# Kernel optimization log

Hardware: AMD Instinct MI355X
Metric: run time of the kernel (lower is better)

Reference implementation:

```python
import jax, jax.numpy as jnp
import numpy as np

B, S, D = 4, 1024, 1024
H = 16
DH = D // H           # 64
ROT = 64              # rotary_emb_dim (full head dim)
NEG_INF = -10000.0
ROPE_BASE = 10000.0


def _rope_tables(seqlen, rot_dim, dtype=jnp.float32):
    inv_freq = 1.0 / (ROPE_BASE ** (jnp.arange(0, rot_dim, 2, dtype=jnp.float32) / rot_dim))
    t = jnp.arange(seqlen, dtype=jnp.float32)
    freqs = jnp.einsum('s,f->sf', t, inv_freq)  # (S, rot_dim//2)
    return jnp.cos(freqs).astype(dtype), jnp.sin(freqs).astype(dtype)


def _apply_rotary(x, cos, sin):
    # x: (B, S, H, DH); GPT-NeoX (non-interleaved) rotary over first ROT dims
    half = ROT // 2
    x_rot, x_pass = x[..., :ROT], x[..., ROT:]
    x1, x2 = x_rot[..., :half], x_rot[..., half:]
    c = cos[None, :, None, :]
    s = sin[None, :, None, :]
    rot = jnp.concatenate([x1 * c - x2 * s, x2 * c + x1 * s], axis=-1)
    return jnp.concatenate([rot, x_pass], axis=-1) if x_pass.shape[-1] else rot


def setup_inputs() -> dict:
    key = jax.random.key(0)
    ks = jax.random.split(key, 5)
    sc_in = 1.0 / np.sqrt(D)
    return {
        'x': jax.random.normal(ks[0], (B, S, D), jnp.float32),
        'Wqkv': jax.random.normal(ks[1], (3 * D, D), jnp.float32) * sc_in,
        'bqkv': jax.random.normal(ks[2], (3 * D,), jnp.float32) * 0.01,
        'Wout': jax.random.normal(ks[3], (D, D), jnp.float32) * sc_in,
        'bout': jax.random.normal(ks[4], (D,), jnp.float32) * 0.01,
    }


def reference(x, Wqkv, bqkv, Wout, bout):
    # QKV projection: (B,S,D) -> (B,S,3,H,DH)
    qkv = (jnp.einsum('bsd,ed->bse', x, Wqkv) + bqkv).reshape(B, S, 3, H, DH)
    q, k, v = qkv[:, :, 0], qkv[:, :, 1], qkv[:, :, 2]
    cos, sin = _rope_tables(S, ROT, q.dtype)
    q = _apply_rotary(q, cos, sin)
    k = _apply_rotary(k, cos, sin)
    scale = 1.0 / np.sqrt(DH)
    scores = jnp.einsum('bthd,bshd->bhts', q, k * scale)  # (B,H,S,S)
    causal_mask = jnp.triu(jnp.full((S, S), NEG_INF, dtype=scores.dtype), 1)
    scores = scores + causal_mask
    attn = jax.nn.softmax(scores, axis=-1)
    out = jnp.einsum('bhts,bshd->bthd', attn, v).reshape(B, S, D)
    return jnp.einsum('bsd,ed->bse', out, Wout) + bout
```

## Files before the change

kernel.cpp:

```cpp
#include <hip/hip_runtime.h>

#define B_ 4
#define S_ 1024
#define D_ 1024
#define H_ 16
#define DH_ 64

typedef unsigned short u16;
typedef __attribute__((ext_vector_type(8))) short bf16x8;
typedef __attribute__((ext_vector_type(4))) float f32x4;

__device__ __forceinline__ float bf2f(u16 h){
  union { unsigned u; float f; } x; x.u = ((unsigned)h) << 16; return x.f;
}
__device__ __forceinline__ u16 f2bf(float f){
  union { float f; unsigned u; } x; x.f = f;
  unsigned u = x.u;
  return (u16)((u + 0x7fffu + ((u >> 16) & 1u)) >> 16);
}

__device__ __forceinline__ void gload16(const u16* g, u16* l){
  __builtin_amdgcn_global_load_lds(
      (const __attribute__((address_space(1))) unsigned int*)g,
      (__attribute__((address_space(3))) unsigned int*)l, 16, 0, 0);
}

__global__ __launch_bounds__(256) void cast3(
    const float* __restrict__ a, u16* __restrict__ oa, int na,
    const float* __restrict__ b, u16* __restrict__ ob, int nb,
    const float* __restrict__ c, u16* __restrict__ oc){
  int i = (blockIdx.x * 256 + threadIdx.x) * 4;
  const float* src; u16* dst;
  if (i < na){ src = a + i; dst = oa + i; }
  else if (i < na + nb){ src = b + (i - na); dst = ob + (i - na); }
  else { src = c + (i - na - nb); dst = oc + (i - na - nb); }
  float4 v = *(const float4*)src;
  union { u16 s[4]; uint2 u; } o;
  o.s[0] = f2bf(v.x); o.s[1] = f2bf(v.y); o.s[2] = f2bf(v.z); o.s[3] = f2bf(v.w);
  *(uint2*)dst = o.u;
}

__global__ __launch_bounds__(256) void rope_tab(float2* __restrict__ tab){
  int idx = blockIdx.x * 256 + threadIdx.x;
  int s = idx >> 5, i = idx & 31;
  float invf = powf(10000.0f, -(float)i * (1.0f / 32.0f));
  float sn, cs;
  sincosf((float)s * invf, &sn, &cs);
  tab[idx] = make_float2(cs, sn);
}

__global__ __launch_bounds__(512, 2) void gemm_qkv8(const u16* __restrict__ A,
    const u16* __restrict__ Bm, const float* __restrict__ bias,
    const float2* __restrict__ tab,
    u16* __restrict__ qb, u16* __restrict__ kb, u16* __restrict__ vb){
  __shared__ u16 As_[2][2][128*64];
  __shared__ u16 Bs_[2][2][128*64];
  const int K = 1024;
  const int tid = threadIdx.x;
  const int lane = tid & 63, wid = tid >> 6;
  const int wr = wid >> 2, wc = wid & 3;
  const int lo = lane & 15, g = lane >> 4;

  const int bid = blockIdx.x;
  const int swz = (bid & 7) * 24 + (bid >> 3);
  const int bx = swz & 15, by = swz >> 4;
  const int m0 = bx * 256, n0 = by * 256;

  f32x4 acc[8][4];
  #pragma unroll
  for (int i = 0; i < 8; ++i)
    #pragma unroll
    for (int j = 0; j < 4; ++j) acc[i][j] = (f32x4){0.f, 0.f, 0.f, 0.f};

  auto stage = [&](int b, int kt){
    const u16* ga = A + (size_t)m0 * K + kt * 64;
    const u16* gb = Bm + (size_t)n0 * K + kt * 64;
    #pragma unroll
    for (int it = 0; it < 2; ++it){
      int c = tid + it * 512;
      int r = c >> 3;
      int colbs = ((c & 7) * 16) ^ ((r & 7) << 4);
      int src = r * K + (colbs >> 1);
      gload16(ga + src,           &As_[b][0][c * 8]);
      gload16(ga + 128*K + src,   &As_[b][1][c * 8]);
      gload16(gb + src,           &Bs_[b][0][c * 8]);
      gload16(gb + 128*K + src,   &Bs_[b][1][c * 8]);
    }
  };

  auto rdA = [&](int b, int qm, int fm, int ks) -> bf16x8 {
    int row = qm*64 + fm*16 + lo;
    int byte = row*128 + ((ks*64 + g*16) ^ ((lo & 7) << 4));
    return *(const bf16x8*)(&As_[b][wr][byte >> 1]);
  };
  auto rdB = [&](int b, int qn, int fn, int ks) -> bf16x8 {
    int row = (wc & 1)*64 + qn*32 + fn*16 + lo;
    int byte = row*128 + ((ks*64 + g*16) ^ ((lo & 7) << 4));
    return *(const bf16x8*)(&Bs_[b][wc >> 1][byte >> 1]);
  };

  auto ktile = [&](int b, int stage_t){
    bf16x8 a[8], bq[4];
    #pragma unroll
    for (int fm = 0; fm < 4; ++fm)
      #pragma unroll
      for (int ks = 0; ks < 2; ++ks) a[fm*2+ks] = rdA(b, 0, fm, ks);
    #pragma unroll
    for (int fn = 0; fn < 2; ++fn)
      #pragma unroll
      for (int ks = 0; ks < 2; ++ks) bq[fn*2+ks] = rdB(b, 0, fn, ks);
    __builtin_amdgcn_s_setprio(1);
    #pragma unroll
    for (int fm = 0; fm < 4; ++fm)
      #pragma unroll
      for (int fn = 0; fn < 2; ++fn)
        #pragma unroll
        for (int ks = 0; ks < 2; ++ks)
          acc[fm][fn] = __builtin_amdgcn_mfma_f32_16x16x32_bf16(a[fm*2+ks], bq[fn*2+ks], acc[fm][fn], 0, 0, 0);
    __builtin_amdgcn_s_setprio(0);
    #pragma unroll
    for (int fn = 0; fn < 2; ++fn)
      #pragma unroll
      for (int ks = 0; ks < 2; ++ks) bq[fn*2+ks] = rdB(b, 1, fn, ks);
    __builtin_amdgcn_s_setprio(1);
    #pragma unroll
    for (int fm = 0; fm < 4; ++fm)
      #pragma unroll
      for (int fn = 0; fn < 2; ++fn)
        #pragma unroll
        for (int ks = 0; ks < 2; ++ks)
          acc[fm][2+fn] = __builtin_amdgcn_mfma_f32_16x16x32_bf16(a[fm*2+ks], bq[fn*2+ks], acc[fm][2+fn], 0, 0, 0);
    __builtin_amdgcn_s_setprio(0);
    #pragma unroll
    for (int fm = 0; fm < 4; ++fm)
      #pragma unroll
      for (int ks = 0; ks < 2; ++ks) a[fm*2+ks] = rdA(b, 1, fm, ks);
    #pragma unroll
    for (int fn = 0; fn < 2; ++fn)
      #pragma unroll
      for (int ks = 0; ks < 2; ++ks) bq[fn*2+ks] = rdB(b, 0, fn, ks);
    __builtin_amdgcn_s_setprio(1);
    #pragma unroll
    for (int fm = 0; fm < 4; ++fm)
      #pragma unroll
      for (int fn = 0; fn < 2; ++fn)
        #pragma unroll
        for (int ks = 0; ks < 2; ++ks)
          acc[4+fm][fn] = __builtin_amdgcn_mfma_f32_16x16x32_bf16(a[fm*2+ks], bq[fn*2+ks], acc[4+fm][fn], 0, 0, 0);
    __builtin_amdgcn_s_setprio(0);
    #pragma unroll
    for (int fn = 0; fn < 2; ++fn)
      #pragma unroll
      for (int ks = 0; ks < 2; ++ks) bq[fn*2+ks] = rdB(b, 1, fn, ks);
    asm volatile("s_waitcnt lgkmcnt(0)" ::: "memory");
    __builtin_amdgcn_sched_barrier(0);
    __builtin_amdgcn_s_barrier();
    __builtin_amdgcn_sched_barrier(0);
    if (stage_t >= 0) stage(b, stage_t);
    __builtin_amdgcn_s_setprio(1);
    #pragma unroll
    for (int fm = 0; fm < 4; ++fm)
      #pragma unroll
      for (int fn = 0; fn < 2; ++fn)
        #pragma unroll
        for (int ks = 0; ks < 2; ++ks)
          acc[4+fm][2+fn] = __builtin_amdgcn_mfma_f32_16x16x32_bf16(a[fm*2+ks], bq[fn*2+ks], acc[4+fm][2+fn], 0, 0, 0);
    __builtin_amdgcn_s_setprio(0);
  };

  stage(0, 0);
  stage(1, 1);
  for (int t = 0; t < 14; ++t){
    asm volatile("s_waitcnt vmcnt(8)" ::: "memory");
    __builtin_amdgcn_s_barrier();
    __builtin_amdgcn_sched_barrier(0);
    ktile(t & 1, t + 2);
  }
  asm volatile("s_waitcnt vmcnt(8)" ::: "memory");
  __builtin_amdgcn_s_barrier();
  __builtin_amdgcn_sched_barrier(0);
  ktile(0, -1);
  asm volatile("s_waitcnt vmcnt(0)" ::: "memory");
  __builtin_amdgcn_s_barrier();
  __builtin_amdgcn_sched_barrier(0);
  ktile(1, -1);

  const int ty = by >> 2;
  const int h  = (by & 3) * 4 + wc;
  float bv[4];
  #pragma unroll
  for (int fn = 0; fn < 4; ++fn) bv[fn] = bias[n0 + wc*64 + fn*16 + lo];

  if (ty < 2){
    u16* dst = (ty == 0) ? qb : kb;
    #pragma unroll
    for (int fm = 0; fm < 8; ++fm){
      #pragma unroll
      for (int j = 0; j < 4; ++j){
        int row = m0 + wr*128 + fm*16 + g*4 + j;
        int bb = row >> 10, s = row & 1023;
        size_t obase = (((size_t)(bb * H_ + h)) * S_ + s) * DH_;
        #pragma unroll
        for (int fn = 0; fn < 2; ++fn){
          int i = fn*16 + lo;
          float2 t2 = tab[s*32 + i];
          float v1 = acc[fm][fn][j] + bv[fn];
          float v2 = acc[fm][fn+2][j] + bv[fn+2];
          dst[obase + i]      = f2bf(v1 * t2.x - v2 * t2.y);
          dst[obase + i + 32] = f2bf(v2 * t2.x + v1 * t2.y);
        }
      }
    }
  } else {
    #pragma unroll
    for (int fm = 0; fm < 8; ++fm){
      #pragma unroll
      for (int j = 0; j < 4; ++j){
        int row = m0 + wr*128 + fm*16 + g*4 + j;
        int bb = row >> 10, s = row & 1023;
        size_t obase = (((size_t)(bb * H_ + h)) * S_ + s) * DH_;
        #pragma unroll
        for (int fn = 0; fn < 4; ++fn)
          vb[obase + fn*16 + lo] = f2bf(acc[fm][fn][j] + bv[fn]);
      }
    }
  }
}

template<int OUT_BF16>
__global__ __launch_bounds__(256) void gemm_bt(const u16* __restrict__ A,
    const u16* __restrict__ Bm, const float* __restrict__ bias,
    void* __restrict__ Cout, int M, int N, int K){
  __shared__ u16 As[2][128*32];
  __shared__ u16 Bs[2][128*32];
  const int tid = threadIdx.x;
  const int lane = tid & 63;
  const int w = tid >> 6;
  const int wr = w >> 1, wc = w & 1;
  const int lo = lane & 15, g = lane >> 4;
  const int m0 = blockIdx.x * 128, n0 = blockIdx.y * 128;

  f32x4 acc[4][4];
  #pragma unroll
  for (int i = 0; i < 4; ++i)
    #pragma unroll
    for (int j = 0; j < 4; ++j) acc[i][j] = (f32x4){0.f, 0.f, 0.f, 0.f};

  const int nt = K >> 5;

  auto stage = [&](int buf, int kt){
    const u16* ga = A + (size_t)m0 * K + kt * 32;
    const u16* gb = Bm + (size_t)n0 * K + kt * 32;
    #pragma unroll
    for (int it = 0; it < 2; ++it){
      int chunk = tid + it * 256;
      int row = chunk >> 2;
      int c0 = (chunk & 3) * 8;
      gload16(ga + (size_t)row * K + c0, &As[buf][chunk * 8]);
      gload16(gb + (size_t)row * K + c0, &Bs[buf][chunk * 8]);
    }
  };

  stage(0, 0);
  __syncthreads();
  int buf = 0;
  for (int kt = 0; kt < nt; ++kt){
    if (kt + 1 < nt) stage(buf ^ 1, kt + 1);
    bf16x8 af[4], bfr[4];
    #pragma unroll
    for (int mi = 0; mi < 4; ++mi)
      af[mi] = *(const bf16x8*)(&As[buf][(wr*64 + mi*16 + lo)*32 + g*8]);
    #pragma unroll
    for (int ni = 0; ni < 4; ++ni)
      bfr[ni] = *(const bf16x8*)(&Bs[buf][(wc*64 + ni*16 + lo)*32 + g*8]);
    #pragma unroll
    for (int mi = 0; mi < 4; ++mi)
      #pragma unroll
      for (int ni = 0; ni < 4; ++ni)
        acc[mi][ni] = __builtin_amdgcn_mfma_f32_16x16x32_bf16(af[mi], bfr[ni], acc[mi][ni], 0, 0, 0);
    __syncthreads();
    buf ^= 1;
  }

  #pragma unroll
  for (int mi = 0; mi < 4; ++mi){
    int row = m0 + wr*64 + mi*16 + g*4;
    #pragma unroll
    for (int ni = 0; ni < 4; ++ni){
      int col = n0 + wc*64 + ni*16 + lo;
      float bvs = bias[col];
      #pragma unroll
      for (int j = 0; j < 4; ++j){
        float v = acc[mi][ni][j] + bvs;
        if (OUT_BF16) ((u16*)Cout)[(size_t)(row + j) * N + col] = f2bf(v);
        else          ((float*)Cout)[(size_t)(row + j) * N + col] = v;
      }
    }
  }
}

__global__ __launch_bounds__(256) void vtrans(const u16* __restrict__ vb,
                                              u16* __restrict__ vtb){
  const int bh = blockIdx.x;
  const int st = blockIdx.y;
  const int t = threadIdx.x;
  __shared__ u16 T[64][72];

  const int sl = t >> 2;
  const int i0 = (t & 3) * 16;
  const u16* src = vb + (((size_t)bh * S_) + st*64 + sl) * DH_ + i0;
  bf16x8 a = *(const bf16x8*)src;
  bf16x8 c = *(const bf16x8*)(src + 8);
  #pragma unroll
  for (int e = 0; e < 8; ++e){
    T[i0 + e][sl]     = (u16)a[e];
    T[i0 + 8 + e][sl] = (u16)c[e];
  }
  __syncthreads();
  const int d = t >> 2;
  const int sc = (t & 3) * 16;
  bf16x8 o1 = *(const bf16x8*)(&T[d][sc]);
  bf16x8 o2 = *(const bf16x8*)(&T[d][sc + 8]);
  size_t vdst = ((size_t)bh * DH_ + d) * S_ + st*64 + sc;
  *(bf16x8*)(vtb + vdst)     = o1;
  *(bf16x8*)(vtb + vdst + 8) = o2;
}

__global__ __launch_bounds__(256) void attn_fwd(const u16* __restrict__ qb,
    const u16* __restrict__ kb, const u16* __restrict__ vtb,
    u16* __restrict__ ctx){
  const int bh = blockIdx.x;
  const int qt = 15 - blockIdx.y;
  const int b = bh >> 4, h = bh & 15;
  const int tid = threadIdx.x;
  const int lane = tid & 63, w = tid >> 6;
  const int lo = lane & 15, g = lane >> 4;

  __shared__ u16 Kl[2][64*64];
  __shared__ u16 Vl[2][64*64];
  __shared__ u16 Plds[4][16][72];

  bf16x8 qf[2];
  {
    const u16* qa = qb + ((size_t)bh * S_ + qt*64 + w*16 + lo) * DH_ + g*8;
    qf[0] = *(const bf16x8*)(qa);  qf[1] = *(const bf16x8*)(qa + 32);
  }

  float m_run[4], l_run[4];
  f32x4 O[4];
  #pragma unroll
  for (int j = 0; j < 4; ++j){ m_run[j] = -1e30f; l_run[j] = 0.f; }
  #pragma unroll
  for (int c = 0; c < 4; ++c) O[c] = (f32x4){0.f,0.f,0.f,0.f};

  auto stage = [&](int buf, int kt){
    const u16* ksrc = kb  + ((size_t)bh * S_ + kt*64) * DH_;
    const u16* vsrc = vtb + (size_t)bh * DH_ * S_ + kt*64;
    #pragma unroll
    for (int it = 0; it < 2; ++it){
      int c = tid + it * 256;
      int row = c >> 3;
      int colb = (c & 7) * 16;
      int colbs = colb ^ ((row & 7) << 4);
      gload16(ksrc + (size_t)row * DH_ + (colbs >> 1), &Kl[buf][c * 8]);
      gload16(vsrc + (size_t)row * S_  + (colbs >> 1), &Vl[buf][c * 8]);
    }
  };

  int buf = 0;

  auto computeTile = [&](bool diag){
    f32x4 sacc[4];
    #pragma unroll
    for (int c = 0; c < 4; ++c) sacc[c] = (f32x4){0.f,0.f,0.f,0.f};
    __builtin_amdgcn_s_setprio(1);
    #pragma unroll
    for (int cf = 0; cf < 4; ++cf){
      int r = cf*16 + lo;
      #pragma unroll
      for (int ks = 0; ks < 2; ++ks){
        int byteoff = r*128 + ((ks*64 + g*16) ^ ((lo & 7) << 4));
        bf16x8 kf = *(const bf16x8*)(&Kl[buf][byteoff >> 1]);
        sacc[cf] = __builtin_amdgcn_mfma_f32_16x16x32_bf16(qf[ks], kf, sacc[cf], 0, 0, 0);
      }
    }
    __builtin_amdgcn_s_setprio(0);
    #pragma unroll
    for (int cf = 0; cf < 4; ++cf){
      #pragma unroll
      for (int j = 0; j < 4; ++j){
        float sv = sacc[cf][j] * 0.125f;
        if (diag){
          int kj = cf*16 + lo;
          int qr = w*16 + g*4 + j;
          if (kj > qr) sv -= 10000.f;
        }
        sacc[cf][j] = sv;
      }
    }
    float mnew[4], alpha[4], rsum[4];
    #pragma unroll
    for (int j = 0; j < 4; ++j){
      float v = fmaxf(fmaxf(sacc[0][j], sacc[1][j]), fmaxf(sacc[2][j], sacc[3][j]));
      v = fmaxf(v, __shfl_xor(v, 1));
      v = fmaxf(v, __shfl_xor(v, 2));
      v = fmaxf(v, __shfl_xor(v, 4));
      v = fmaxf(v, __shfl_xor(v, 8));
      mnew[j] = fmaxf(m_run[j], v);
      alpha[j] = __expf(m_run[j] - mnew[j]);
      m_run[j] = mnew[j];
      rsum[j] = 0.f;
    }
    #pragma unroll
    for (int cf = 0; cf < 4; ++cf){
      #pragma unroll
      for (int j = 0; j < 4; ++j){
        float pv = __expf(sacc[cf][j] - mnew[j]);
        sacc[cf][j] = pv;
        rsum[j] += pv;
      }
    }
    #pragma unroll
    for (int j = 0; j < 4; ++j){
      float v = rsum[j];
      v += __shfl_xor(v, 1);
      v += __shfl_xor(v, 2);
      v += __shfl_xor(v, 4);
      v += __shfl_xor(v, 8);
      l_run[j] = l_run[j] * alpha[j] + v;
    }
    #pragma unroll
    for (int c = 0; c < 4; ++c)
      #pragma unroll
      for (int j = 0; j < 4; ++j) O[c][j] *= alpha[j];

    #pragma unroll
    for (int cf = 0; cf < 4; ++cf)
      #pragma unroll
      for (int j = 0; j < 4; ++j)
        Plds[w][g*4 + j][cf*16 + lo] = f2bf(sacc[cf][j]);

    __builtin_amdgcn_s_setprio(1);
    #pragma unroll
    for (int ks = 0; ks < 2; ++ks){
      bf16x8 pf = *(const bf16x8*)(&Plds[w][lo][ks*32 + g*8]);
      #pragma unroll
      for (int ocf = 0; ocf < 4; ++ocf){
        int r = ocf*16 + lo;
        int byteoff = r*128 + ((ks*64 + g*16) ^ ((lo & 7) << 4));
        bf16x8 vf = *(const bf16x8*)(&Vl[buf][byteoff >> 1]);
        O[ocf] = __builtin_amdgcn_mfma_f32_16x16x32_bf16(pf, vf, O[ocf], 0, 0, 0);
      }
    }
    __builtin_amdgcn_s_setprio(0);
  };

  stage(0, 0);
  for (int kt = 0; kt <= qt; ++kt){
    __syncthreads();
    if (kt < qt) stage(buf ^ 1, kt + 1);
    computeTile(kt == qt);
    buf ^= 1;
  }

  float inv[4];
  #pragma unroll
  for (int j = 0; j < 4; ++j) inv[j] = 1.0f / l_run[j];
  #pragma unroll
  for (int ocf = 0; ocf < 4; ++ocf){
    #pragma unroll
    for (int j = 0; j < 4; ++j){
      int d = ocf*16 + lo;
      int qi = qt*64 + w*16 + g*4 + j;
      ctx[((size_t)(b * S_ + qi)) * D_ + h * DH_ + d] = f2bf(O[ocf][j] * inv[j]);
    }
  }
}

extern "C" void kernel_launch(void* const* d_in, const int* in_sizes, int n_in,
                              void* d_out, int out_size, void* d_ws, size_t ws_size,
                              hipStream_t stream){
  (void)in_sizes; (void)n_in; (void)out_size; (void)ws_size;
  const float* x    = (const float*)d_in[0];
  const float* Wqkv = (const float*)d_in[1];
  const float* bqkv = (const float*)d_in[2];
  const float* Wout = (const float*)d_in[3];
  const float* bout = (const float*)d_in[4];
  float* out = (float*)d_out;

  char* p = (char*)d_ws;
  u16* x_bf    = (u16*)p; p += (size_t)4096*1024*2;
  u16* wqkv_bf = (u16*)p; p += (size_t)3072*1024*2;
  u16* wout_bf = (u16*)p; p += (size_t)1024*1024*2;
  u16* q_bf    = (u16*)p; p += (size_t)4096*1024*2;
  u16* k_bf    = (u16*)p; p += (size_t)4096*1024*2;
  u16* v_bf    = (u16*)p; p += (size_t)4096*1024*2;
  u16* vt_bf   = (u16*)p; p += (size_t)4096*1024*2;
  u16* ctx_bf  = (u16*)p; p += (size_t)4096*1024*2;
  float2* tab  = (float2*)p; p += (size_t)1024*32*8;

  const int na = 4096*1024, nb = 3072*1024;
  cast3<<<8192, 256, 0, stream>>>(x, x_bf, na, Wqkv, wqkv_bf, nb, Wout, wout_bf);
  rope_tab<<<128, 256, 0, stream>>>(tab);

  gemm_qkv8<<<192, 512, 0, stream>>>(x_bf, wqkv_bf, bqkv, tab, q_bf, k_bf, v_bf);

  vtrans<<<dim3(64, 16), 256, 0, stream>>>(v_bf, vt_bf);

  attn_fwd<<<dim3(64, 16), 256, 0, stream>>>(q_bf, k_bf, vt_bf, ctx_bf);

  gemm_bt<0><<<dim3(32, 8), 256, 0, stream>>>(ctx_bf, wout_bf, bout, out, 4096, 1024, 1024);
}
```

Baseline: 113.4 us.

## Fuse V transpose into QKV GEMM epilogue and enlarge attention query tiles

```diff
diff --git a/kernel.cpp b/kernel.cpp
--- a/kernel.cpp
+++ b/kernel.cpp
@@ -52,7 +52,7 @@
 __global__ __launch_bounds__(512, 2) void gemm_qkv8(const u16* __restrict__ A,
     const u16* __restrict__ Bm, const float* __restrict__ bias,
     const float2* __restrict__ tab,
-    u16* __restrict__ qb, u16* __restrict__ kb, u16* __restrict__ vb){
+    u16* __restrict__ qb, u16* __restrict__ kb, u16* __restrict__ vtb){
   __shared__ u16 As_[2][2][128*64];
   __shared__ u16 Bs_[2][2][128*64];
   const int K = 1024;
@@ -93,22 +93,22 @@
     int byte = row*128 + ((ks*64 + g*16) ^ ((lo & 7) << 4));
     return *(const bf16x8*)(&As_[b][wr][byte >> 1]);
   };
-  auto rdB = [&](int b, int qn, int fn, int ks) -> bf16x8 {
-    int row = (wc & 1)*64 + qn*32 + fn*16 + lo;
+  auto rdB = [&](int b, int fn, int ks) -> bf16x8 {
+    int row = (wc & 1)*64 + fn*16 + lo;
     int byte = row*128 + ((ks*64 + g*16) ^ ((lo & 7) << 4));
     return *(const bf16x8*)(&Bs_[b][wc >> 1][byte >> 1]);
   };
 
   auto ktile = [&](int b, int stage_t){
-    bf16x8 a[8], bq[4];
+    bf16x8 a[8], bq[8];
     #pragma unroll
     for (int fm = 0; fm < 4; ++fm)
       #pragma unroll
       for (int ks = 0; ks < 2; ++ks) a[fm*2+ks] = rdA(b, 0, fm, ks);
     #pragma unroll
-    for (int fn = 0; fn < 2; ++fn)
-      #pragma unroll
-      for (int ks = 0; ks < 2; ++ks) bq[fn*2+ks] = rdB(b, 0, fn, ks);
+    for (int fn = 0; fn < 4; ++fn)
+      #pragma unroll
+      for (int ks = 0; ks < 2; ++ks) bq[fn*2+ks] = rdB(b, fn, ks);
     __builtin_amdgcn_s_setprio(1);
     #pragma unroll
     for (int fm = 0; fm < 4; ++fm)
@@ -118,10 +118,6 @@
         for (int ks = 0; ks < 2; ++ks)
           acc[fm][fn] = __builtin_amdgcn_mfma_f32_16x16x32_bf16(a[fm*2+ks], bq[fn*2+ks], acc[fm][fn], 0, 0, 0);
     __builtin_amdgcn_s_setprio(0);
-    #pragma unroll
-    for (int fn = 0; fn < 2; ++fn)
-      #pragma unroll
-      for (int ks = 0; ks < 2; ++ks) bq[fn*2+ks] = rdB(b, 1, fn, ks);
     __builtin_amdgcn_s_setprio(1);
     #pragma unroll
     for (int fm = 0; fm < 4; ++fm)
@@ -129,16 +125,12 @@
       for (int fn = 0; fn < 2; ++fn)
         #pragma unroll
         for (int ks = 0; ks < 2; ++ks)
-          acc[fm][2+fn] = __builtin_amdgcn_mfma_f32_16x16x32_bf16(a[fm*2+ks], bq[fn*2+ks], acc[fm][2+fn], 0, 0, 0);
+          acc[fm][2+fn] = __builtin_amdgcn_mfma_f32_16x16x32_bf16(a[fm*2+ks], bq[(2+fn)*2+ks], acc[fm][2+fn], 0, 0, 0);
     __builtin_amdgcn_s_setprio(0);
     #pragma unroll
     for (int fm = 0; fm < 4; ++fm)
       #pragma unroll
       for (int ks = 0; ks < 2; ++ks) a[fm*2+ks] = rdA(b, 1, fm, ks);
-    #pragma unroll
-    for (int fn = 0; fn < 2; ++fn)
-      #pragma unroll
-      for (int ks = 0; ks < 2; ++ks) bq[fn*2+ks] = rdB(b, 0, fn, ks);
     __builtin_amdgcn_s_setprio(1);
     #pragma unroll
     for (int fm = 0; fm < 4; ++fm)
@@ -148,10 +140,6 @@
         for (int ks = 0; ks < 2; ++ks)
           acc[4+fm][fn] = __builtin_amdgcn_mfma_f32_16x16x32_bf16(a[fm*2+ks], bq[fn*2+ks], acc[4+fm][fn], 0, 0, 0);
     __builtin_amdgcn_s_setprio(0);
-    #pragma unroll
-    for (int fn = 0; fn < 2; ++fn)
-      #pragma unroll
-      for (int ks = 0; ks < 2; ++ks) bq[fn*2+ks] = rdB(b, 1, fn, ks);
     asm volatile("s_waitcnt lgkmcnt(0)" ::: "memory");
     __builtin_amdgcn_sched_barrier(0);
     __builtin_amdgcn_s_barrier();
@@ -164,7 +152,7 @@
       for (int fn = 0; fn < 2; ++fn)
         #pragma unroll
         for (int ks = 0; ks < 2; ++ks)
-          acc[4+fm][2+fn] = __builtin_amdgcn_mfma_f32_16x16x32_bf16(a[fm*2+ks], bq[fn*2+ks], acc[4+fm][2+fn], 0, 0, 0);
+          acc[4+fm][2+fn] = __builtin_amdgcn_mfma_f32_16x16x32_bf16(a[fm*2+ks], bq[(2+fn)*2+ks], acc[4+fm][2+fn], 0, 0, 0);
     __builtin_amdgcn_s_setprio(0);
   };
 
@@ -212,17 +200,31 @@
       }
     }
   } else {
-    #pragma unroll
-    for (int fm = 0; fm < 8; ++fm){
-      #pragma unroll
-      for (int j = 0; j < 4; ++j){
-        int row = m0 + wr*128 + fm*16 + g*4 + j;
-        int bb = row >> 10, s = row & 1023;
-        size_t obase = (((size_t)(bb * H_ + h)) * S_ + s) * DH_;
-        #pragma unroll
-        for (int fn = 0; fn < 4; ++fn)
-          vb[obase + fn*16 + lo] = f2bf(acc[fm][fn][j] + bv[fn]);
-      }
+    __syncthreads();
+    u16* wbase = (wid < 4) ? ((u16*)As_ + wid * 8192)
+                           : ((u16*)Bs_ + (wid - 4) * 8192);
+    #pragma unroll
+    for (int fm = 0; fm < 8; ++fm)
+      #pragma unroll
+      for (int fn = 0; fn < 4; ++fn){
+        int d = fn*16 + lo;
+        #pragma unroll
+        for (int j = 0; j < 4; ++j){
+          int sl = fm*16 + g*4 + j;
+          int sx = sl ^ ((d & 7) << 4);
+          wbase[d*128 + sx] = f2bf(acc[fm][fn][j] + bv[fn]);
+        }
+      }
+    const int rowblk = m0 + wr*128;
+    const int bb = rowblk >> 10;
+    const int sbase = rowblk & 1023;
+    #pragma unroll
+    for (int pass = 0; pass < 16; ++pass){
+      int d = pass*4 + g;
+      int sc = lo * 8;
+      int sx = sc ^ ((d & 7) << 4);
+      bf16x8 v = *(const bf16x8*)(&wbase[d*128 + sx]);
+      *(bf16x8*)(vtb + (((size_t)(bb * H_ + h)) * DH_ + d) * S_ + sbase + sc) = v;
     }
   }
 }
@@ -299,38 +301,11 @@
   }
 }
 
-__global__ __launch_bounds__(256) void vtrans(const u16* __restrict__ vb,
-                                              u16* __restrict__ vtb){
-  const int bh = blockIdx.x;
-  const int st = blockIdx.y;
-  const int t = threadIdx.x;
-  __shared__ u16 T[64][72];
-
-  const int sl = t >> 2;
-  const int i0 = (t & 3) * 16;
-  const u16* src = vb + (((size_t)bh * S_) + st*64 + sl) * DH_ + i0;
-  bf16x8 a = *(const bf16x8*)src;
-  bf16x8 c = *(const bf16x8*)(src + 8);
-  #pragma unroll
-  for (int e = 0; e < 8; ++e){
-    T[i0 + e][sl]     = (u16)a[e];
-    T[i0 + 8 + e][sl] = (u16)c[e];
-  }
-  __syncthreads();
-  const int d = t >> 2;
-  const int sc = (t & 3) * 16;
-  bf16x8 o1 = *(const bf16x8*)(&T[d][sc]);
-  bf16x8 o2 = *(const bf16x8*)(&T[d][sc + 8]);
-  size_t vdst = ((size_t)bh * DH_ + d) * S_ + st*64 + sc;
-  *(bf16x8*)(vtb + vdst)     = o1;
-  *(bf16x8*)(vtb + vdst + 8) = o2;
-}
-
-__global__ __launch_bounds__(256) void attn_fwd(const u16* __restrict__ qb,
+__global__ __launch_bounds__(512) void attn_fwd(const u16* __restrict__ qb,
     const u16* __restrict__ kb, const u16* __restrict__ vtb,
     u16* __restrict__ ctx){
   const int bh = blockIdx.x;
-  const int qt = 15 - blockIdx.y;
+  const int qt = 7 - blockIdx.y;
   const int b = bh >> 4, h = bh & 15;
   const int tid = threadIdx.x;
   const int lane = tid & 63, w = tid >> 6;
@@ -338,11 +313,11 @@
 
   __shared__ u16 Kl[2][64*64];
   __shared__ u16 Vl[2][64*64];
-  __shared__ u16 Plds[4][16][72];
+  __shared__ u16 Plds[8][16][72];
 
   bf16x8 qf[2];
   {
-    const u16* qa = qb + ((size_t)bh * S_ + qt*64 + w*16 + lo) * DH_ + g*8;
+    const u16* qa = qb + ((size_t)bh * S_ + qt*128 + w*16 + lo) * DH_ + g*8;
     qf[0] = *(const bf16x8*)(qa);  qf[1] = *(const bf16x8*)(qa + 32);
   }
 
@@ -356,20 +331,16 @@
   auto stage = [&](int buf, int kt){
     const u16* ksrc = kb  + ((size_t)bh * S_ + kt*64) * DH_;
     const u16* vsrc = vtb + (size_t)bh * DH_ * S_ + kt*64;
-    #pragma unroll
-    for (int it = 0; it < 2; ++it){
-      int c = tid + it * 256;
-      int row = c >> 3;
-      int colb = (c & 7) * 16;
-      int colbs = colb ^ ((row & 7) << 4);
-      gload16(ksrc + (size_t)row * DH_ + (colbs >> 1), &Kl[buf][c * 8]);
-      gload16(vsrc + (size_t)row * S_  + (colbs >> 1), &Vl[buf][c * 8]);
-    }
+    int c = tid;
+    int row = c >> 3;
+    int colbs = ((c & 7) * 16) ^ ((row & 7) << 4);
+    gload16(ksrc + (size_t)row * DH_ + (colbs >> 1), &Kl[buf][c * 8]);
+    gload16(vsrc + (size_t)row * S_  + (colbs >> 1), &Vl[buf][c * 8]);
   };
 
   int buf = 0;
 
-  auto computeTile = [&](bool diag){
+  auto computeTile = [&](int kt, bool diag){
     f32x4 sacc[4];
     #pragma unroll
     for (int c = 0; c < 4; ++c) sacc[c] = (f32x4){0.f,0.f,0.f,0.f};
@@ -391,8 +362,8 @@
       for (int j = 0; j < 4; ++j){
         float sv = sacc[cf][j] * 0.125f;
         if (diag){
-          int kj = cf*16 + lo;
-          int qr = w*16 + g*4 + j;
+          int kj = kt*64 + cf*16 + lo;
+          int qr = qt*128 + w*16 + g*4 + j;
           if (kj > qr) sv -= 10000.f;
         }
         sacc[cf][j] = sv;
@@ -455,11 +426,12 @@
     __builtin_amdgcn_s_setprio(0);
   };
 
+  const int nsteps = 2*qt + 2;
   stage(0, 0);
-  for (int kt = 0; kt <= qt; ++kt){
+  for (int kt = 0; kt < nsteps; ++kt){
     __syncthreads();
-    if (kt < qt) stage(buf ^ 1, kt + 1);
-    computeTile(kt == qt);
+    if (kt + 1 < nsteps) stage(buf ^ 1, kt + 1);
+    computeTile(kt, kt >= 2*qt);
     buf ^= 1;
   }
 
@@ -471,7 +443,7 @@
     #pragma unroll
     for (int j = 0; j < 4; ++j){
       int d = ocf*16 + lo;
-      int qi = qt*64 + w*16 + g*4 + j;
+      int qi = qt*128 + w*16 + g*4 + j;
       ctx[((size_t)(b * S_ + qi)) * D_ + h * DH_ + d] = f2bf(O[ocf][j] * inv[j]);
     }
   }
@@ -494,7 +466,6 @@
   u16* wout_bf = (u16*)p; p += (size_t)1024*1024*2;
   u16* q_bf    = (u16*)p; p += (size_t)4096*1024*2;
   u16* k_bf    = (u16*)p; p += (size_t)4096*1024*2;
-  u16* v_bf    = (u16*)p; p += (size_t)4096*1024*2;
   u16* vt_bf   = (u16*)p; p += (size_t)4096*1024*2;
   u16* ctx_bf  = (u16*)p; p += (size_t)4096*1024*2;
   float2* tab  = (float2*)p; p += (size_t)1024*32*8;
@@ -503,11 +474,9 @@
   cast3<<<8192, 256, 0, stream>>>(x, x_bf, na, Wqkv, wqkv_bf, nb, Wout, wout_bf);
   rope_tab<<<128, 256, 0, stream>>>(tab);
 
-  gemm_qkv8<<<192, 512, 0, stream>>>(x_bf, wqkv_bf, bqkv, tab, q_bf, k_bf, v_bf);
-
-  vtrans<<<dim3(64, 16), 256, 0, stream>>>(v_bf, vt_bf);
-
-  attn_fwd<<<dim3(64, 16), 256, 0, stream>>>(q_bf, k_bf, vt_bf, ctx_bf);
+  gemm_qkv8<<<192, 512, 0, stream>>>(x_bf, wqkv_bf, bqkv, tab, q_bf, k_bf, vt_bf);
+
+  attn_fwd<<<dim3(64, 8), 512, 0, stream>>>(q_bf, k_bf, vt_bf, ctx_bf);
 
   gemm_bt<0><<<dim3(32, 8), 256, 0, stream>>>(ctx_bf, wout_bf, bout, out, 4096, 1024, 1024);
 }
```

Measured after the change: 113.0 us. Within noise of the previous version (-0.3%).
